# Kernel tuning notes

Measured on AMD Instinct MI355X. Metric: run time of the kernel, lower is better.

The kernel has to match this reference:

```python
import jax, jax.numpy as jnp
import numpy as np

B, L, C = 4, 2048, 512
D_STATE, D_CONV, EXPAND = 16, 4, 2
D_INNER = EXPAND * C
DT_RANK = C // 16  # mamba_ssm 'auto' dt_rank


def setup_inputs() -> dict:
    key = jax.random.key(0)
    ks = jax.random.split(key, 12)
    s = 0.02
    p = {}
    p["x"] = jax.random.normal(ks[0], (B, L, C), jnp.float32)
    p["gamma1"] = jnp.ones((C,), jnp.float32)
    p["beta1"] = jnp.zeros((C,), jnp.float32)
    # leading dim 2 = (forward mamba, backward mamba)
    p["W_in"] = jax.random.normal(ks[1], (2, 2 * D_INNER, C), jnp.float32) * s
    p["conv_w"] = jax.random.normal(ks[2], (2, D_INNER, D_CONV), jnp.float32) * s
    p["conv_b"] = jnp.zeros((2, D_INNER), jnp.float32)
    p["W_xproj"] = jax.random.normal(ks[3], (2, DT_RANK + 2 * D_STATE, D_INNER), jnp.float32) * s
    p["W_dt"] = jax.random.normal(ks[4], (2, D_INNER, DT_RANK), jnp.float32) * s
    p["b_dt"] = jax.random.normal(ks[5], (2, D_INNER), jnp.float32) * s
    p["A_log"] = jnp.tile(jnp.log(jnp.arange(1, D_STATE + 1, dtype=jnp.float32))[None, None, :], (2, D_INNER, 1))
    p["Dp"] = jnp.ones((2, D_INNER), jnp.float32)
    p["W_out"] = jax.random.normal(ks[6], (2, C, D_INNER), jnp.float32) * s
    p["gamma2"] = jnp.ones((C,), jnp.float32)
    p["beta2"] = jnp.zeros((C,), jnp.float32)
    p["W1"] = jax.random.normal(ks[7], (4 * C, C), jnp.float32) * s
    p["b1"] = jnp.zeros((4 * C,), jnp.float32)
    p["W2"] = jax.random.normal(ks[8], (C, 4 * C), jnp.float32) * s
    p["b2"] = jnp.zeros((C,), jnp.float32)
    return p


def layer_norm(x, g, b, eps=1e-5):
    mu = x.mean(-1, keepdims=True)
    var = ((x - mu) ** 2).mean(-1, keepdims=True)
    return (x - mu) * jax.lax.rsqrt(var + eps) * g + b


def mamba_one(x, W_in, conv_w, conv_b, W_xproj, W_dt, b_dt, A_log, Dv, W_out):
    # x: [B, L, C] -> [B, L, C]; faithful to mamba_ssm Mamba (in_proj no bias,
    # depthwise causal conv1d with bias, x_proj no bias, dt_proj with bias, out_proj no bias)
    u, z = jnp.split(x @ W_in.T, 2, axis=-1)          # [B,L,d_inner] each
    uc = jnp.pad(u.transpose(0, 2, 1), ((0, 0), (0, 0), (D_CONV - 1, 0)))  # causal pad
    uc = jax.lax.conv_general_dilated(uc, conv_w[:, None, :], (1,), 'VALID',
                                      feature_group_count=D_INNER)
    u = jax.nn.silu((uc + conv_b[None, :, None]).transpose(0, 2, 1))       # [B,L,d_inner]
    x_dbl = u @ W_xproj.T                              # [B,L,dt_rank+2*d_state]
    dt = jax.nn.softplus(x_dbl[..., :DT_RANK] @ W_dt.T + b_dt)             # [B,L,d_inner]
    Bm = x_dbl[..., DT_RANK:DT_RANK + D_STATE]         # [B,L,d_state]
    Cm = x_dbl[..., DT_RANK + D_STATE:]                # [B,L,d_state]
    A = -jnp.exp(A_log)                                # [d_inner,d_state]

    def step(h, ins):
        dt_t, B_t, C_t, u_t = ins                      # [B,d],[B,s],[B,s],[B,d]
        h = jnp.exp(dt_t[..., None] * A) * h + (dt_t * u_t)[..., None] * B_t[:, None, :]
        return h, jnp.einsum('bds,bs->bd', h, C_t)

    h0 = jnp.zeros((x.shape[0], D_INNER, D_STATE), x.dtype)
    xs = (dt.transpose(1, 0, 2), Bm.transpose(1, 0, 2), Cm.transpose(1, 0, 2), u.transpose(1, 0, 2))
    _, ys = jax.lax.scan(step, h0, xs)                 # ys: [L,B,d_inner]
    y = ys.transpose(1, 0, 2) + u * Dv
    y = y * jax.nn.silu(z)
    return y @ W_out.T


def reference(x, gamma1, beta1, W_in, conv_w, conv_b, W_xproj, W_dt, b_dt,
              A_log, Dp, W_out, gamma2, beta2, W1, b1, W2, b2):
    xn = layer_norm(x, gamma1, beta1)
    x2 = jnp.stack([xn, jnp.flip(xn, axis=1)])         # [2,B,L,C]
    ys = jax.vmap(mamba_one)(x2, W_in, conv_w, conv_b, W_xproj, W_dt, b_dt, A_log, Dp, W_out)
    y = (ys[0] + jnp.flip(ys[1], axis=1)) * 0.5
    x = x + y                                          # residual (dropout=0)
    h = jax.nn.gelu(layer_norm(x, gamma2, beta2) @ W1.T + b1, approximate=False)
    return x + (h @ W2.T + b2)
```

## Files before the change

### kernel.cpp

```cpp
#include <hip/hip_runtime.h>
#include <math.h>

#define B_ 4
#define L_ 2048
#define C_ 512
#define DI 1024
#define DS 16
#define NTOK 8192
#define SLICE ((long)NTOK * DI)
#define T_ 64
#define NC_ 32
#define SDT_LD 264

typedef __attribute__((ext_vector_type(4))) float  f32x4;
typedef __attribute__((ext_vector_type(4))) short  s16x4;
typedef __attribute__((ext_vector_type(8))) short  s16x8;
typedef __attribute__((ext_vector_type(8))) __bf16 bf16x8;

#define LOG2E 1.4426950408889634f
#define LN2   0.69314718055994531f

__device__ __forceinline__ float bf2f(short s) {
  return __uint_as_float(((unsigned)(unsigned short)s) << 16);
}
__device__ __forceinline__ short f2bf(float f) {
  unsigned u = __float_as_uint(f);
  u += 0x7fffu + ((u >> 16) & 1u);
  return (short)(u >> 16);
}
__device__ __forceinline__ f32x4 mfma16(s16x8 a, s16x8 b, f32x4 c) {
  return __builtin_amdgcn_mfma_f32_16x16x32_bf16(
      __builtin_bit_cast(bf16x8, a), __builtin_bit_cast(bf16x8, b), c, 0, 0, 0);
}
__device__ __forceinline__ float fast_sigmoid(float z) {
  return __builtin_amdgcn_rcpf(1.f + __builtin_amdgcn_exp2f(-LOG2E * z));
}
__device__ __forceinline__ float fast_softplus(float t) {
  return (t > 15.f) ? t
    : LN2 * __builtin_amdgcn_logf(1.f + __builtin_amdgcn_exp2f(LOG2E * t));
}

__global__ __launch_bounds__(256) void castw_kernel(const float* __restrict__ s,
                                                    short* __restrict__ d, int n) {
  int i = (blockIdx.x * 256 + threadIdx.x) * 4;
  if (i >= n) return;
  f32x4 v = *(const f32x4*)(s + i);
  s16x4 o;
#pragma unroll
  for (int k = 0; k < 4; ++k) o[k] = f2bf(v[k]);
  *(s16x4*)(d + i) = o;
}

__global__ __launch_bounds__(256) void ln1_kernel(
    const float* __restrict__ x, const float* __restrict__ g,
    const float* __restrict__ bt, short* __restrict__ out)
{
  int tok  = blockIdx.x * 4 + (threadIdx.x >> 6);
  int lane = threadIdx.x & 63;
  const float* row = x + (long)tok * C_ + lane * 8;
  f32x4 a0 = *(const f32x4*)row, a1 = *(const f32x4*)(row + 4);
  float s = 0.f, q = 0.f;
#pragma unroll
  for (int i = 0; i < 4; ++i) { s += a0[i] + a1[i]; q += a0[i]*a0[i] + a1[i]*a1[i]; }
#pragma unroll
  for (int o = 1; o < 64; o <<= 1) { s += __shfl_xor(s, o); q += __shfl_xor(q, o); }
  float mu = s * (1.f / C_);
  float rs = rsqrtf(q * (1.f / C_) - mu * mu + 1e-5f);
  f32x4 g0 = *(const f32x4*)(g + lane*8), g1 = *(const f32x4*)(g + lane*8 + 4);
  f32x4 b0 = *(const f32x4*)(bt + lane*8), b1 = *(const f32x4*)(bt + lane*8 + 4);
  s16x8 o8;
#pragma unroll
  for (int i = 0; i < 4; ++i) {
    o8[i]     = f2bf((a0[i] - mu) * rs * g0[i] + b0[i]);
    o8[4 + i] = f2bf((a1[i] - mu) * rs * g1[i] + b1[i]);
  }
  *(s16x8*)(out + (long)tok * C_ + lane * 8) = o8;
}

__global__ __launch_bounds__(256) void combine_ln2_kernel(
    const float* __restrict__ x, const float* __restrict__ yo,
    const float* __restrict__ g, const float* __restrict__ bt,
    float* __restrict__ xmid, short* __restrict__ xln)
{
  int tok  = blockIdx.x * 4 + (threadIdx.x >> 6);
  int lane = threadIdx.x & 63;
  long base = (long)tok * C_ + lane * 8;
  f32x4 a0 = *(const f32x4*)(x + base),  a1 = *(const f32x4*)(x + base + 4);
  f32x4 p0 = *(const f32x4*)(yo + base), p1 = *(const f32x4*)(yo + base + 4);
  f32x4 q0 = *(const f32x4*)(yo + (long)NTOK * C_ + base);
  f32x4 q1 = *(const f32x4*)(yo + (long)NTOK * C_ + base + 4);
  a0 = a0 + 0.5f * (p0 + q0);
  a1 = a1 + 0.5f * (p1 + q1);
  *(f32x4*)(xmid + base) = a0;
  *(f32x4*)(xmid + base + 4) = a1;
  float s = 0.f, q = 0.f;
#pragma unroll
  for (int i = 0; i < 4; ++i) { s += a0[i] + a1[i]; q += a0[i]*a0[i] + a1[i]*a1[i]; }
#pragma unroll
  for (int o = 1; o < 64; o <<= 1) { s += __shfl_xor(s, o); q += __shfl_xor(q, o); }
  float mu = s * (1.f / C_);
  float rs = rsqrtf(q * (1.f / C_) - mu * mu + 1e-5f);
  f32x4 g0 = *(const f32x4*)(g + lane*8), g1 = *(const f32x4*)(g + lane*8 + 4);
  f32x4 b0 = *(const f32x4*)(bt + lane*8), b1 = *(const f32x4*)(bt + lane*8 + 4);
  s16x8 o8;
#pragma unroll
  for (int i = 0; i < 4; ++i) {
    o8[i]     = f2bf((a0[i] - mu) * rs * g0[i] + b0[i]);
    o8[4 + i] = f2bf((a1[i] - mu) * rs * g1[i] + b1[i]);
  }
  *(s16x8*)(xln + (long)tok * C_ + lane * 8) = o8;
}

__global__ __launch_bounds__(256) void conv_silu_kernel(
    const short* __restrict__ ubuf, const float* __restrict__ cw,
    const float* __restrict__ cb, short* __restrict__ ucv)
{
  int ch = blockIdx.x * 256 + threadIdx.x;
  int tc = blockIdx.y;
  int db = blockIdx.z;
  int d = db >> 2, b = db & 3;
  const short* U = ubuf + ((long)d * NTOK + (long)b * L_) * DI + ch;
  short* O = ucv + ((long)d * NTOK + (long)b * L_) * DI + ch;
  f32x4 w4 = *(const f32x4*)(cw + ((long)d * DI + ch) * 4);
  float bias = cb[d * DI + ch];
  int t0 = tc * 128;
  if (d == 0) {
    float h3 = (t0 >= 3) ? bf2f(U[(long)(t0 - 3) * DI]) : 0.f;
    float h2 = (t0 >= 2) ? bf2f(U[(long)(t0 - 2) * DI]) : 0.f;
    float h1 = (t0 >= 1) ? bf2f(U[(long)(t0 - 1) * DI]) : 0.f;
    for (int t = t0; t < t0 + 128; ++t) {
      float cur = bf2f(U[(long)t * DI]);
      float v = w4[0]*h3 + w4[1]*h2 + w4[2]*h1 + w4[3]*cur + bias;
      v = v * fast_sigmoid(v);
      O[(long)t * DI] = f2bf(v);
      h3 = h2; h2 = h1; h1 = cur;
    }
  } else {
    float a0v = bf2f(U[(long)t0 * DI]);
    float a1v = (t0 + 1 < L_) ? bf2f(U[(long)(t0 + 1) * DI]) : 0.f;
    float a2v = (t0 + 2 < L_) ? bf2f(U[(long)(t0 + 2) * DI]) : 0.f;
    for (int t = t0; t < t0 + 128; ++t) {
      float a3v = (t + 3 < L_) ? bf2f(U[(long)(t + 3) * DI]) : 0.f;
      float v = w4[3]*a0v + w4[2]*a1v + w4[1]*a2v + w4[0]*a3v + bias;
      v = v * fast_sigmoid(v);
      O[(long)t * DI] = f2bf(v);
      a0v = a1v; a1v = a2v; a2v = a3v;
    }
  }
}

template <int PASS, int DIR>
__global__ __launch_bounds__(256) void scan_pass(
    const short* __restrict__ dtr, const short* __restrict__ wdt,
    const float* __restrict__ bdt,
    const short* __restrict__ ucv, const float* __restrict__ xdbl,
    const short* __restrict__ zbuf,
    const float* __restrict__ Alog, const float* __restrict__ Dp,
    float* __restrict__ hbuf, float* __restrict__ Sbuf, short* __restrict__ ybuf)
{
  __shared__ float sBC[T_ * 32];
  __shared__ short sdt[T_ * SDT_LD];
  const int tid  = threadIdx.x;
  const int lane = tid & 63;
  const int w    = tid >> 6;
  const int ch   = blockIdx.x * 256 + tid;
  const int c    = blockIdx.y;
  const int b    = blockIdx.z;
  const int db   = DIR * 4 + b;
  const long n0  = (long)b * L_ + (long)c * T_;
  const float* xrow = xdbl + ((long)DIR * NTOK + n0) * 64 + 32;
  if (PASS == 0) {
    int r = tid >> 2, cc4 = (tid & 3) * 4;
    *(f32x4*)&sBC[r * 16 + cc4] = *(const f32x4*)(xrow + (long)r * 64 + cc4);
  } else {
    int r = tid >> 2, cc8 = (tid & 3) * 8;
    *(f32x4*)&sBC[r * 32 + cc8]     = *(const f32x4*)(xrow + (long)r * 64 + cc8);
    *(f32x4*)&sBC[r * 32 + cc8 + 4] = *(const f32x4*)(xrow + (long)r * 64 + cc8 + 4);
  }
  {
    const short* dtrp = dtr + ((long)DIR * NTOK + n0) * 32;
    const short* wp   = wdt + ((long)DIR * DI + blockIdx.x * 256) * 32;
    s16x8 af[4], bfr[4];
#pragma unroll
    for (int mi = 0; mi < 4; ++mi)
      af[mi] = *(const s16x8*)(dtrp + (mi * 16 + (lane & 15)) * 32 + (lane >> 4) * 8);
#pragma unroll
    for (int ni = 0; ni < 4; ++ni)
      bfr[ni] = *(const s16x8*)(wp + (w * 64 + ni * 16 + (lane & 15)) * 32 + (lane >> 4) * 8);
    float bv[4];
#pragma unroll
    for (int ni = 0; ni < 4; ++ni)
      bv[ni] = bdt[DIR * DI + blockIdx.x * 256 + w * 64 + ni * 16 + (lane & 15)];
#pragma unroll
    for (int mi = 0; mi < 4; ++mi) {
#pragma unroll
      for (int ni = 0; ni < 4; ++ni) {
        f32x4 acc = {0.f, 0.f, 0.f, 0.f};
        acc = mfma16(af[mi], bfr[ni], acc);
#pragma unroll
        for (int j = 0; j < 4; ++j) {
          float sp = fast_softplus(acc[j] + bv[ni]);
          sdt[(mi * 16 + (lane >> 4) * 4 + j) * SDT_LD + w * 64 + ni * 16 + (lane & 15)]
            = f2bf(sp);
        }
      }
    }
  }
  __syncthreads();
  float A2[16];
  {
    const float* Ap = Alog + ((long)DIR * DI + ch) * DS;
#pragma unroll
    for (int s = 0; s < 16; ++s) A2[s] = -expf(Ap[s]) * LOG2E;
  }
  const long base = ((long)DIR * NTOK + n0) * DI + ch;
  const short* up  = ucv + base;
  const short* zp  = zbuf + base;
  short* yp = ybuf + base;
  const long hb = (((long)db * NC_ + c) * DI + ch) * 16;
  float h[16];
  float Dv = 0.f;
  if (PASS == 1) {
#pragma unroll
    for (int s = 0; s < 16; s += 4) *(f32x4*)&h[s] = *(const f32x4*)&hbuf[hb + s];
    Dv = Dp[DIR * DI + ch];
  } else {
#pragma unroll
    for (int s = 0; s < 16; ++s) h[s] = 0.f;
  }
  float S = 0.f;
#pragma unroll
  for (int ib = 0; ib < T_ / 8; ++ib) {
    const int t0 = DIR ? (T_ - 8 - ib * 8) : ib * 8;
    float u8[8], z8[8];
#pragma unroll
    for (int j = 0; j < 8; ++j) {
      long o = (long)(t0 + j) * DI;
      u8[j] = bf2f(up[o]);
      if (PASS == 1) z8[j] = bf2f(zp[o]);
    }
    short y8[8];
#pragma unroll
    for (int jj = 0; jj < 8; ++jj) {
      const int j = DIR ? (7 - jj) : jj;
      float dtv = bf2f(sdt[(t0 + j) * SDT_LD + tid]);
      float uv  = u8[j];
      float wv = dtv * uv;
      const float* bc = &sBC[(t0 + j) * (PASS ? 32 : 16)];
      float p = 0.f;
#pragma unroll
      for (int s = 0; s < 16; ++s) {
        float e = __builtin_amdgcn_exp2f(dtv * A2[s]);
        h[s] = e * h[s] + wv * bc[s];
        if (PASS == 1) p += h[s] * bc[16 + s];
      }
      if (PASS == 0) {
        S += dtv;
      } else {
        float z = z8[j];
        y8[j] = f2bf((p + uv * Dv) * (z * fast_sigmoid(z)));
      }
    }
    if (PASS == 1) {
#pragma unroll
      for (int j = 0; j < 8; ++j) yp[(long)(t0 + j) * DI] = y8[j];
    }
  }
  if (PASS == 0) {
#pragma unroll
    for (int s = 0; s < 16; s += 4) *(f32x4*)&hbuf[hb + s] = *(const f32x4*)&h[s];
    Sbuf[((long)db * NC_ + c) * DI + ch] = S;
  }
}

__global__ __launch_bounds__(256) void scan_combine(
    const float* __restrict__ Alog, float* __restrict__ hbuf,
    const float* __restrict__ Sbuf)
{
  int tid = threadIdx.x;
  int ch = (blockIdx.x & 3) * 256 + tid;
  int db = blockIdx.x >> 2;
  int d = db >> 2;
  float A2[16];
  const float* Ap = Alog + ((long)d * DI + ch) * DS;
#pragma unroll
  for (int s = 0; s < 16; ++s) A2[s] = -expf(Ap[s]) * LOG2E;
  float h[16];
#pragma unroll
  for (int s = 0; s < 16; ++s) h[s] = 0.f;
  for (int cc = 0; cc < NC_; ++cc) {
    int c = (d == 1) ? (NC_ - 1 - cc) : cc;
    long hb = (((long)db * NC_ + c) * DI + ch) * 16;
    float S = Sbuf[((long)db * NC_ + c) * DI + ch];
    float he[16];
#pragma unroll
    for (int s = 0; s < 16; s += 4) *(f32x4*)&he[s] = *(const f32x4*)&hbuf[hb + s];
#pragma unroll
    for (int s = 0; s < 16; s += 4) *(f32x4*)&hbuf[hb + s] = *(const f32x4*)&h[s];
#pragma unroll
    for (int s = 0; s < 16; ++s) h[s] = __builtin_amdgcn_exp2f(A2[s] * S) * h[s] + he[s];
  }
}

template <int EPI, int BN>
__global__ __launch_bounds__(256) void gemm_m97(
    const short* __restrict__ X, long sX,
    const short* __restrict__ Wb, long sW,
    const float* __restrict__ bias, long sBias,
    float* __restrict__ outF, long sOutF,
    short* __restrict__ outB,
    const float* __restrict__ res,
    short* __restrict__ outB2,
    int K, int N)
{
  constexpr int MI = (BN == 128) ? 4 : 2;
  __shared__ short sA[128 * 32];
  __shared__ short sB[BN * 32];
  const int tid  = threadIdx.x;
  const int lane = tid & 63;
  const int w    = tid >> 6;
  const int wm   = (BN == 128) ? (w >> 1) : w;
  const int wn   = (BN == 128) ? (w & 1) : 0;
  const int d    = blockIdx.z;
  const int m0   = blockIdx.x * 128;
  const int n0   = blockIdx.y * BN;
  const short* Xp = X + (long)d * sX + (long)m0 * K;
  const short* Wp = Wb + (long)d * sW + (long)n0 * K;

  f32x4 acc[MI][4];
#pragma unroll
  for (int i = 0; i < MI; ++i)
#pragma unroll
    for (int j = 0; j < 4; ++j) acc[i][j] = (f32x4){0.f, 0.f, 0.f, 0.f};

  const int lrow = lane >> 2;
  const int lkg  = lane & 3;

  for (int k0 = 0; k0 < K; k0 += 32) {
#pragma unroll
    for (int j = 0; j < 2; ++j) {
      int row = w * 16 + j * 64 + lrow;
      int kgs = lkg ^ ((row >> 1) & 3);
      __builtin_amdgcn_global_load_lds(
        (const __attribute__((address_space(1))) unsigned*)(Xp + (long)row * K + k0 + kgs * 8),
        (__attribute__((address_space(3))) unsigned*)(sA + (w * 16 + j * 64) * 32),
        16, 0, 0);
    }
#pragma unroll
    for (int j = 0; j < BN / 64; ++j) {
      int row = w * 16 + j * 64 + lrow;
      int kgs = lkg ^ ((row >> 1) & 3);
      __builtin_amdgcn_global_load_lds(
        (const __attribute__((address_space(1))) unsigned*)(Wp + (long)row * K + k0 + kgs * 8),
        (__attribute__((address_space(3))) unsigned*)(sB + (w * 16 + j * 64) * 32),
        16, 0, 0);
    }
    __syncthreads();
    s16x8 af[MI], bfr[4];
#pragma unroll
    for (int mi = 0; mi < MI; ++mi) {
      int row = wm * (MI * 16) + mi * 16 + (lane & 15);
      int kg = (lane >> 4) ^ ((row >> 1) & 3);
      af[mi] = *(const s16x8*)((const char*)sA + row * 64 + kg * 16);
    }
#pragma unroll
    for (int ni = 0; ni < 4; ++ni) {
      int row = wn * 64 + ni * 16 + (lane & 15);
      int kg = (lane >> 4) ^ ((row >> 1) & 3);
      bfr[ni] = *(const s16x8*)((const char*)sB + row * 64 + kg * 16);
    }
#pragma unroll
    for (int mi = 0; mi < MI; ++mi)
#pragma unroll
      for (int ni = 0; ni < 4; ++ni)
        acc[mi][ni] = mfma16(af[mi], bfr[ni], acc[mi][ni]);
    __syncthreads();
  }

  const int col0 = lane & 15;
  const int rsub = (lane >> 4) * 4;
#pragma unroll
  for (int mi = 0; mi < MI; ++mi) {
    int row = m0 + wm * (MI * 16) + mi * 16 + rsub;
#pragma unroll
    for (int ni = 0; ni < 4; ++ni) {
      int col = n0 + wn * 64 + ni * 16 + col0;
#pragma unroll
      for (int j = 0; j < 4; ++j) {
        float v = acc[mi][ni][j];
        int r = row + j;
        if constexpr (EPI == 0) {
          outF[(long)d * sOutF + (long)r * N + col] = v;
        } else if constexpr (EPI == 1) {
          int d2 = col >> 11, cc = col & 2047;
          long o = ((long)d2 * NTOK + r) * DI;
          if (cc < DI) outB[o + cc] = f2bf(v);
          else         outB2[o + cc - DI] = f2bf(v);
        } else if constexpr (EPI == 3) {
          float t = v + bias[col];
          float u3 = t * (1.f + 0.044715f * t * t);
          float sg = __builtin_amdgcn_rcpf(1.f + __builtin_amdgcn_exp2f(-2.3022083f * u3));
          outB[(long)r * N + col] = f2bf(t * sg);
        } else if constexpr (EPI == 4) {
          outF[(long)r * N + col] = v + bias[col] + res[(long)r * N + col];
        } else if constexpr (EPI == 5) {
          if (col < 32) outB[((long)d * NTOK + r) * 32 + col] = f2bf(v);
          else          outF[((long)d * NTOK + r) * 64 + col] = v;
        }
      }
    }
  }
}

extern "C" void kernel_launch(void* const* d_in, const int* in_sizes, int n_in,
                              void* d_out, int out_size, void* d_ws, size_t ws_size,
                              hipStream_t stream) {
  const float* x      = (const float*)d_in[0];
  const float* gamma1 = (const float*)d_in[1];
  const float* beta1  = (const float*)d_in[2];
  const float* W_in   = (const float*)d_in[3];
  const float* conv_w = (const float*)d_in[4];
  const float* conv_b = (const float*)d_in[5];
  const float* W_xprj = (const float*)d_in[6];
  const float* W_dt   = (const float*)d_in[7];
  const float* b_dt   = (const float*)d_in[8];
  const float* A_log  = (const float*)d_in[9];
  const float* Dp     = (const float*)d_in[10];
  const float* W_out  = (const float*)d_in[11];
  const float* gamma2 = (const float*)d_in[12];
  const float* beta2  = (const float*)d_in[13];
  const float* W1     = (const float*)d_in[14];
  const float* b1     = (const float*)d_in[15];
  const float* W2     = (const float*)d_in[16];
  const float* b2     = (const float*)d_in[17];
  float* out = (float*)d_out;

  char* ws = (char*)d_ws;
  short* wb_in  = (short*)(ws);
  short* wb_xp  = (short*)(ws + (4L << 20));
  short* wb_dt  = (short*)(ws + (4L << 20) + (256L << 10));
  short* wb_out = (short*)(ws + (4L << 20) + (384L << 10));
  short* wb_w1  = (short*)(ws + (6L << 20) + (384L << 10));
  short* wb_w2  = (short*)(ws + (8L << 20) + (384L << 10));
  short* xnbf = (short*)(ws + (12L << 20));
  short* ubuf = (short*)(ws + (20L << 20));
  short* zbuf = (short*)(ws + (52L << 20));
  short* ucv  = (short*)(ws + (84L << 20));
  short* Hbuf = (short*)(ws + (116L << 20));
  float* xdbl = (float*)(ws + (148L << 20));
  short* dtr  = (short*)(ws + (152L << 20));
  float* hbuf = (float*)(ws + (153L << 20));
  float* Sbuf = (float*)(ws + (169L << 20));
  float* xmid = (float*)(ws + (170L << 20));
  float* yo   = (float*)zbuf;
  short* xln  = xnbf;

  castw_kernel<<<2048, 256, 0, stream>>>(W_in,   wb_in,  2097152);
  castw_kernel<<<128,  256, 0, stream>>>(W_xprj, wb_xp,  131072);
  castw_kernel<<<64,   256, 0, stream>>>(W_dt,   wb_dt,  65536);
  castw_kernel<<<1024, 256, 0, stream>>>(W_out,  wb_out, 1048576);
  castw_kernel<<<1024, 256, 0, stream>>>(W1,     wb_w1,  1048576);
  castw_kernel<<<1024, 256, 0, stream>>>(W2,     wb_w2,  1048576);
  ln1_kernel<<<NTOK / 4, 256, 0, stream>>>(x, gamma1, beta1, xnbf);
  gemm_m97<1, 128><<<dim3(64, 32, 1), 256, 0, stream>>>(
      xnbf, 0, wb_in, 0, nullptr, 0, nullptr, 0, ubuf, nullptr, zbuf, C_, 4096);
  conv_silu_kernel<<<dim3(4, 16, 8), 256, 0, stream>>>(ubuf, conv_w, conv_b, ucv);
  gemm_m97<5, 64><<<dim3(64, 1, 2), 256, 0, stream>>>(
      ucv, SLICE, wb_xp, 64L * DI, nullptr, 0, xdbl, 0, dtr, nullptr, nullptr, DI, 64);
  scan_pass<0, 0><<<dim3(4, NC_, 4), 256, 0, stream>>>(dtr, wb_dt, b_dt, ucv, xdbl, zbuf, A_log, Dp, hbuf, Sbuf, ucv);
  scan_pass<0, 1><<<dim3(4, NC_, 4), 256, 0, stream>>>(dtr, wb_dt, b_dt, ucv, xdbl, zbuf, A_log, Dp, hbuf, Sbuf, ucv);
  scan_combine<<<32, 256, 0, stream>>>(A_log, hbuf, Sbuf);
  scan_pass<1, 0><<<dim3(4, NC_, 4), 256, 0, stream>>>(dtr, wb_dt, b_dt, ucv, xdbl, zbuf, A_log, Dp, hbuf, Sbuf, ucv);
  scan_pass<1, 1><<<dim3(4, NC_, 4), 256, 0, stream>>>(dtr, wb_dt, b_dt, ucv, xdbl, zbuf, A_log, Dp, hbuf, Sbuf, ucv);
  gemm_m97<0, 128><<<dim3(64, 4, 2), 256, 0, stream>>>(
      ucv, SLICE, wb_out, (long)C_ * DI, nullptr, 0, yo, (long)NTOK * C_, nullptr,
      nullptr, nullptr, DI, C_);
  combine_ln2_kernel<<<NTOK / 4, 256, 0, stream>>>(x, yo, gamma2, beta2, xmid, xln);
  gemm_m97<3, 128><<<dim3(64, 16, 1), 256, 0, stream>>>(
      xln, 0, wb_w1, 0, b1, 0, nullptr, 0, Hbuf, nullptr, nullptr, C_, 2048);
  gemm_m97<4, 128><<<dim3(64, 4, 1), 256, 0, stream>>>(
      Hbuf, 0, wb_w2, 0, b2, 0, out, 0, nullptr, xmid, nullptr, 2048, C_);
}
```

Baseline: 419.5 us.

## Merge weight casts and scan directions, shrink GEMM tiles, store out-proj in bf16

Folds the six weight-cast launches into one kernel and runs both scan directions in a single launch per pass, with the direction taken from blockIdx.z. Adds a BM template parameter so the x-proj, out-proj and FFN2 GEMMs use 64-row tiles and launch more blocks. The out-proj result is written as bf16 instead of fp32, roughly halving that intermediate's traffic into combine_ln2. f2bf now uses the compiler's native bf16 conversion. The goals are fewer launches and better occupancy on the small GEMMs, at the cost of some precision in the residual branch and a runtime branch on direction inside the scan.

Result: slower. 471.5 us (+12.4%).

```diff
diff --git a/kernel.cpp b/kernel.cpp
--- a/kernel.cpp
+++ b/kernel.cpp
@@ -24,9 +24,7 @@
   return __uint_as_float(((unsigned)(unsigned short)s) << 16);
 }
 __device__ __forceinline__ short f2bf(float f) {
-  unsigned u = __float_as_uint(f);
-  u += 0x7fffu + ((u >> 16) & 1u);
-  return (short)(u >> 16);
+  return __builtin_bit_cast(short, (__bf16)f);
 }
 __device__ __forceinline__ f32x4 mfma16(s16x8 a, s16x8 b, f32x4 c) {
   return __builtin_amdgcn_mfma_f32_16x16x32_bf16(
@@ -40,10 +38,23 @@
     : LN2 * __builtin_amdgcn_logf(1.f + __builtin_amdgcn_exp2f(LOG2E * t));
 }
 
-__global__ __launch_bounds__(256) void castw_kernel(const float* __restrict__ s,
-                                                    short* __restrict__ d, int n) {
-  int i = (blockIdx.x * 256 + threadIdx.x) * 4;
-  if (i >= n) return;
+__global__ __launch_bounds__(256) void castw_all(
+    const float* __restrict__ s0, short* __restrict__ d0,
+    const float* __restrict__ s1, short* __restrict__ d1,
+    const float* __restrict__ s2, short* __restrict__ d2,
+    const float* __restrict__ s3, short* __restrict__ d3,
+    const float* __restrict__ s4, short* __restrict__ d4,
+    const float* __restrict__ s5, short* __restrict__ d5)
+{
+  int b = blockIdx.x;
+  const float* s; short* d; int off;
+  if      (b < 2048) { s = s0; d = d0; off = b; }
+  else if (b < 2176) { s = s1; d = d1; off = b - 2048; }
+  else if (b < 2240) { s = s2; d = d2; off = b - 2176; }
+  else if (b < 3264) { s = s3; d = d3; off = b - 2240; }
+  else if (b < 4288) { s = s4; d = d4; off = b - 3264; }
+  else               { s = s5; d = d5; off = b - 4288; }
+  int i = (off * 256 + threadIdx.x) * 4;
   f32x4 v = *(const f32x4*)(s + i);
   s16x4 o;
 #pragma unroll
@@ -78,7 +89,7 @@
 }
 
 __global__ __launch_bounds__(256) void combine_ln2_kernel(
-    const float* __restrict__ x, const float* __restrict__ yo,
+    const float* __restrict__ x, const short* __restrict__ yob,
     const float* __restrict__ g, const float* __restrict__ bt,
     float* __restrict__ xmid, short* __restrict__ xln)
 {
@@ -86,11 +97,13 @@
   int lane = threadIdx.x & 63;
   long base = (long)tok * C_ + lane * 8;
   f32x4 a0 = *(const f32x4*)(x + base),  a1 = *(const f32x4*)(x + base + 4);
-  f32x4 p0 = *(const f32x4*)(yo + base), p1 = *(const f32x4*)(yo + base + 4);
-  f32x4 q0 = *(const f32x4*)(yo + (long)NTOK * C_ + base);
-  f32x4 q1 = *(const f32x4*)(yo + (long)NTOK * C_ + base + 4);
-  a0 = a0 + 0.5f * (p0 + q0);
-  a1 = a1 + 0.5f * (p1 + q1);
+  s16x8 p8 = *(const s16x8*)(yob + base);
+  s16x8 q8 = *(const s16x8*)(yob + (long)NTOK * C_ + base);
+#pragma unroll
+  for (int i = 0; i < 4; ++i) {
+    a0[i] += 0.5f * (bf2f(p8[i]) + bf2f(q8[i]));
+    a1[i] += 0.5f * (bf2f(p8[4 + i]) + bf2f(q8[4 + i]));
+  }
   *(f32x4*)(xmid + base) = a0;
   *(f32x4*)(xmid + base + 4) = a1;
   float s = 0.f, q = 0.f;
@@ -149,7 +162,7 @@
   }
 }
 
-template <int PASS, int DIR>
+template <int PASS>
 __global__ __launch_bounds__(256) void scan_pass(
     const short* __restrict__ dtr, const short* __restrict__ wdt,
     const float* __restrict__ bdt,
@@ -165,10 +178,10 @@
   const int w    = tid >> 6;
   const int ch   = blockIdx.x * 256 + tid;
   const int c    = blockIdx.y;
-  const int b    = blockIdx.z;
-  const int db   = DIR * 4 + b;
+  const int db   = blockIdx.z;
+  const int d    = db >> 2, b = db & 3;
   const long n0  = (long)b * L_ + (long)c * T_;
-  const float* xrow = xdbl + ((long)DIR * NTOK + n0) * 64 + 32;
+  const float* xrow = xdbl + ((long)d * NTOK + n0) * 64 + 32;
   if (PASS == 0) {
     int r = tid >> 2, cc4 = (tid & 3) * 4;
     *(f32x4*)&sBC[r * 16 + cc4] = *(const f32x4*)(xrow + (long)r * 64 + cc4);
@@ -178,8 +191,8 @@
     *(f32x4*)&sBC[r * 32 + cc8 + 4] = *(const f32x4*)(xrow + (long)r * 64 + cc8 + 4);
   }
   {
-    const short* dtrp = dtr + ((long)DIR * NTOK + n0) * 32;
-    const short* wp   = wdt + ((long)DIR * DI + blockIdx.x * 256) * 32;
+    const short* dtrp = dtr + ((long)d * NTOK + n0) * 32;
+    const short* wp   = wdt + ((long)d * DI + blockIdx.x * 256) * 32;
     s16x8 af[4], bfr[4];
 #pragma unroll
     for (int mi = 0; mi < 4; ++mi)
@@ -190,7 +203,7 @@
     float bv[4];
 #pragma unroll
     for (int ni = 0; ni < 4; ++ni)
-      bv[ni] = bdt[DIR * DI + blockIdx.x * 256 + w * 64 + ni * 16 + (lane & 15)];
+      bv[ni] = bdt[d * DI + blockIdx.x * 256 + w * 64 + ni * 16 + (lane & 15)];
 #pragma unroll
     for (int mi = 0; mi < 4; ++mi) {
 #pragma unroll
@@ -209,11 +222,11 @@
   __syncthreads();
   float A2[16];
   {
-    const float* Ap = Alog + ((long)DIR * DI + ch) * DS;
+    const float* Ap = Alog + ((long)d * DI + ch) * DS;
 #pragma unroll
     for (int s = 0; s < 16; ++s) A2[s] = -expf(Ap[s]) * LOG2E;
   }
-  const long base = ((long)DIR * NTOK + n0) * DI + ch;
+  const long base = ((long)d * NTOK + n0) * DI + ch;
   const short* up  = ucv + base;
   const short* zp  = zbuf + base;
   short* yp = ybuf + base;
@@ -223,7 +236,7 @@
   if (PASS == 1) {
 #pragma unroll
     for (int s = 0; s < 16; s += 4) *(f32x4*)&h[s] = *(const f32x4*)&hbuf[hb + s];
-    Dv = Dp[DIR * DI + ch];
+    Dv = Dp[d * DI + ch];
   } else {
 #pragma unroll
     for (int s = 0; s < 16; ++s) h[s] = 0.f;
@@ -231,7 +244,7 @@
   float S = 0.f;
 #pragma unroll
   for (int ib = 0; ib < T_ / 8; ++ib) {
-    const int t0 = DIR ? (T_ - 8 - ib * 8) : ib * 8;
+    const int t0 = d ? (T_ - 8 - ib * 8) : ib * 8;
     float u8[8], z8[8];
 #pragma unroll
     for (int j = 0; j < 8; ++j) {
@@ -242,7 +255,7 @@
     short y8[8];
 #pragma unroll
     for (int jj = 0; jj < 8; ++jj) {
-      const int j = DIR ? (7 - jj) : jj;
+      const int j = d ? (7 - jj) : jj;
       float dtv = bf2f(sdt[(t0 + j) * SDT_LD + tid]);
       float uv  = u8[j];
       float wv = dtv * uv;
@@ -302,7 +315,7 @@
   }
 }
 
-template <int EPI, int BN>
+template <int EPI, int BM, int BN>
 __global__ __launch_bounds__(256) void gemm_m97(
     const short* __restrict__ X, long sX,
     const short* __restrict__ Wb, long sW,
@@ -313,16 +326,18 @@
     short* __restrict__ outB2,
     int K, int N)
 {
-  constexpr int MI = (BN == 128) ? 4 : 2;
-  __shared__ short sA[128 * 32];
+  constexpr int NWN = BN / 64;
+  constexpr int NWM = 4 / NWN;
+  constexpr int MI  = BM / (16 * NWM);
+  __shared__ short sA[BM * 32];
   __shared__ short sB[BN * 32];
   const int tid  = threadIdx.x;
   const int lane = tid & 63;
   const int w    = tid >> 6;
-  const int wm   = (BN == 128) ? (w >> 1) : w;
-  const int wn   = (BN == 128) ? (w & 1) : 0;
+  const int wm   = (NWN == 2) ? (w >> 1) : w;
+  const int wn   = (NWN == 2) ? (w & 1) : 0;
   const int d    = blockIdx.z;
-  const int m0   = blockIdx.x * 128;
+  const int m0   = blockIdx.x * BM;
   const int n0   = blockIdx.y * BN;
   const short* Xp = X + (long)d * sX + (long)m0 * K;
   const short* Wp = Wb + (long)d * sW + (long)n0 * K;
@@ -338,7 +353,7 @@
 
   for (int k0 = 0; k0 < K; k0 += 32) {
 #pragma unroll
-    for (int j = 0; j < 2; ++j) {
+    for (int j = 0; j < BM / 64; ++j) {
       int row = w * 16 + j * 64 + lrow;
       int kgs = lkg ^ ((row >> 1) & 3);
       __builtin_amdgcn_global_load_lds(
@@ -406,6 +421,8 @@
         } else if constexpr (EPI == 5) {
           if (col < 32) outB[((long)d * NTOK + r) * 32 + col] = f2bf(v);
           else          outF[((long)d * NTOK + r) * 64 + col] = v;
+        } else if constexpr (EPI == 6) {
+          outB[((long)d * NTOK + r) * N + col] = f2bf(v);
         }
       }
     }
@@ -452,32 +469,26 @@
   float* hbuf = (float*)(ws + (153L << 20));
   float* Sbuf = (float*)(ws + (169L << 20));
   float* xmid = (float*)(ws + (170L << 20));
-  float* yo   = (float*)zbuf;
+  short* ybf  = zbuf;
   short* xln  = xnbf;
 
-  castw_kernel<<<2048, 256, 0, stream>>>(W_in,   wb_in,  2097152);
-  castw_kernel<<<128,  256, 0, stream>>>(W_xprj, wb_xp,  131072);
-  castw_kernel<<<64,   256, 0, stream>>>(W_dt,   wb_dt,  65536);
-  castw_kernel<<<1024, 256, 0, stream>>>(W_out,  wb_out, 1048576);
-  castw_kernel<<<1024, 256, 0, stream>>>(W1,     wb_w1,  1048576);
-  castw_kernel<<<1024, 256, 0, stream>>>(W2,     wb_w2,  1048576);
+  castw_all<<<5312, 256, 0, stream>>>(W_in, wb_in, W_xprj, wb_xp, W_dt, wb_dt,
+                                      W_out, wb_out, W1, wb_w1, W2, wb_w2);
   ln1_kernel<<<NTOK / 4, 256, 0, stream>>>(x, gamma1, beta1, xnbf);
-  gemm_m97<1, 128><<<dim3(64, 32, 1), 256, 0, stream>>>(
+  gemm_m97<1, 128, 128><<<dim3(64, 32, 1), 256, 0, stream>>>(
       xnbf, 0, wb_in, 0, nullptr, 0, nullptr, 0, ubuf, nullptr, zbuf, C_, 4096);
   conv_silu_kernel<<<dim3(4, 16, 8), 256, 0, stream>>>(ubuf, conv_w, conv_b, ucv);
-  gemm_m97<5, 64><<<dim3(64, 1, 2), 256, 0, stream>>>(
+  gemm_m97<5, 64, 64><<<dim3(128, 1, 2), 256, 0, stream>>>(
       ucv, SLICE, wb_xp, 64L * DI, nullptr, 0, xdbl, 0, dtr, nullptr, nullptr, DI, 64);
-  scan_pass<0, 0><<<dim3(4, NC_, 4), 256, 0, stream>>>(dtr, wb_dt, b_dt, ucv, xdbl, zbuf, A_log, Dp, hbuf, Sbuf, ucv);
-  scan_pass<0, 1><<<dim3(4, NC_, 4), 256, 0, stream>>>(dtr, wb_dt, b_dt, ucv, xdbl, zbuf, A_log, Dp, hbuf, Sbuf, ucv);
+  scan_pass<0><<<dim3(4, NC_, 8), 256, 0, stream>>>(dtr, wb_dt, b_dt, ucv, xdbl, zbuf, A_log, Dp, hbuf, Sbuf, ucv);
   scan_combine<<<32, 256, 0, stream>>>(A_log, hbuf, Sbuf);
-  scan_pass<1, 0><<<dim3(4, NC_, 4), 256, 0, stream>>>(dtr, wb_dt, b_dt, ucv, xdbl, zbuf, A_log, Dp, hbuf, Sbuf, ucv);
-  scan_pass<1, 1><<<dim3(4, NC_, 4), 256, 0, stream>>>(dtr, wb_dt, b_dt, ucv, xdbl, zbuf, A_log, Dp, hbuf, Sbuf, ucv);
-  gemm_m97<0, 128><<<dim3(64, 4, 2), 256, 0, stream>>>(
-      ucv, SLICE, wb_out, (long)C_ * DI, nullptr, 0, yo, (long)NTOK * C_, nullptr,
+  scan_pass<1><<<dim3(4, NC_, 8), 256, 0, stream>>>(dtr, wb_dt, b_dt, ucv, xdbl, zbuf, A_log, Dp, hbuf, Sbuf, ucv);
+  gemm_m97<6, 64, 128><<<dim3(128, 4, 2), 256, 0, stream>>>(
+      ucv, SLICE, wb_out, (long)C_ * DI, nullptr, 0, nullptr, 0, ybf,
       nullptr, nullptr, DI, C_);
-  combine_ln2_kernel<<<NTOK / 4, 256, 0, stream>>>(x, yo, gamma2, beta2, xmid, xln);
-  gemm_m97<3, 128><<<dim3(64, 16, 1), 256, 0, stream>>>(
+  combine_ln2_kernel<<<NTOK / 4, 256, 0, stream>>>(x, ybf, gamma2, beta2, xmid, xln);
+  gemm_m97<3, 128, 128><<<dim3(64, 16, 1), 256, 0, stream>>>(
       xln, 0, wb_w1, 0, b1, 0, nullptr, 0, Hbuf, nullptr, nullptr, C_, 2048);
-  gemm_m97<4, 128><<<dim3(64, 4, 1), 256, 0, stream>>>(
+  gemm_m97<4, 64, 128><<<dim3(128, 4, 1), 256, 0, stream>>>(
       Hbuf, 0, wb_w2, 0, b2, 0, out, 0, nullptr, xmid, nullptr, 2048, C_);
 }
```
